# Performance work log

Measured on AMD Instinct MI355X. Metric: run time of the kernel, lower is better.

## Reference

```python
import jax, jax.numpy as jnp
import numpy as np

IN_DIM, OUT_DIM, NUM_KNOTS = 256, 256, 20
X_MIN, X_MAX = -5.0, 5.0
H = (X_MAX - X_MIN) / (NUM_KNOTS - 1)  # uniform knot spacing


def setup_inputs() -> dict:
    key = jax.random.key(0)
    k1, k2 = jax.random.split(key, 2)
    x = jax.random.normal(k1, (1024, IN_DIM), dtype=jnp.float32) * 2.0
    # per-(out,in)-pair cubic coefficients for each of the NUM_KNOTS-1 intervals: [a,b,c,d]
    coeffs = jax.random.normal(k2, (OUT_DIM, IN_DIM, NUM_KNOTS - 1, 4), dtype=jnp.float32) * 0.1
    bias = jnp.zeros((OUT_DIM,), dtype=jnp.float32)
    return {"x": x, "coeffs": coeffs, "bias": bias}


def reference(x, coeffs, bias):
    # x: [B, I]; coeffs: [J, I, K, 4]; bias: [J]
    B, I = x.shape
    K = coeffs.shape[2]
    # locate knot interval (clamped -> linear-cubic extrapolation at edges)
    idx = jnp.clip(jnp.floor((x - X_MIN) / H).astype(jnp.int32), 0, K - 1)  # [B, I]
    t = x - (X_MIN + idx.astype(x.dtype) * H)                               # [B, I]
    # gather per-pair interval coefficients: [J, B, I, 4]
    i_arr = jnp.broadcast_to(jnp.arange(I)[None, :], idx.shape)
    c = coeffs[:, i_arr, idx]
    a, b, c2, d = c[..., 0], c[..., 1], c[..., 2], c[..., 3]
    # Horner evaluation; t broadcasts [B,I] -> [J,B,I]
    y = ((d * t + c2) * t + b) * t + a
    # sum over input dims, add bias: [B, J]
    return y.sum(axis=-1).T + bias[None, :]
```

## Files before the change

### kernel.cpp

```cpp
#include <hip/hip_runtime.h>

#define IN_DIM   256
#define OUT_DIM  256
#define NKNOT    19
#define NCOL     (IN_DIM * NKNOT)
#define CPQ      1216
#define SLICE_U4 (CPQ * 64)
#define X_MIN_C  (-5.0f)
#define H_C      (10.0f / 19.0f)
#define INV_H_C  (19.0f / 10.0f)

typedef __fp16 half2_t __attribute__((ext_vector_type(2)));

__device__ __forceinline__ unsigned int pk_f16(float x, float y) {
    return __builtin_bit_cast(unsigned int, __builtin_amdgcn_cvt_pkrtz(x, y));
}

__device__ __forceinline__ float fdot2(unsigned int w, unsigned int c, float acc) {
#if __has_builtin(__builtin_amdgcn_fdot2)
    return __builtin_amdgcn_fdot2(__builtin_bit_cast(half2_t, w),
                                  __builtin_bit_cast(half2_t, c), acc, false);
#else
    half2_t a = __builtin_bit_cast(half2_t, w);
    half2_t b = __builtin_bit_cast(half2_t, c);
    return acc + (float)a.x * (float)b.x + (float)a.y * (float)b.y;
#endif
}

__global__ __launch_bounds__(256) void transpose_pack(
        const float4* __restrict__ src, uint4* __restrict__ dst) {
    __shared__ uint2 tile[64][65];
    const int c0 = (blockIdx.x % 76) * 64;
    const int r0 = (blockIdx.x / 76) * 64;
    const int tx = threadIdx.x & 63;
    const int ty = threadIdx.x >> 6;

    #pragma unroll
    for (int jj = 0; jj < 16; ++jj) {
        const int r = ty * 16 + jj;
        const float4 v = src[(size_t)(r0 + r) * NCOL + (size_t)(c0 + tx)];
        uint2 p;
        p.x = pk_f16(v.x, v.y);
        p.y = pk_f16(v.z, v.w);
        tile[tx][r] = p;
    }
    __syncthreads();

    const int quarter  = c0 / CPQ;
    const int clbase   = c0 - quarter * CPQ;
    const int o_half   = r0 >> 7;
    const int og2_base = (r0 & 127) >> 1;
    uint4* base = dst + (size_t)(quarter * 2 + o_half) * SLICE_U4;

    #pragma unroll
    for (int jj = 0; jj < 8; ++jj) {
        const int p     = jj * 256 + threadIdx.x;
        const int cl    = p >> 5;
        const int og2l  = p & 31;
        const uint2 t0  = tile[cl][og2l * 2];
        const uint2 t1  = tile[cl][og2l * 2 + 1];
        base[(size_t)(clbase + cl) * 64 + og2_base + og2l] =
            make_uint4(t0.x, t0.y, t1.x, t1.y);
    }
}

__global__ __launch_bounds__(256, 4) void kan_partial(
        const float* __restrict__ x,
        const uint4* __restrict__ Ct,
        float2*      __restrict__ part,
        int B) {
    __shared__ int4 s_tk[4 * 64];

    const int s       = blockIdx.x & 7;
    const int o_half  = s & 1;
    const int quarter = s >> 1;
    const int bgrp    = blockIdx.x >> 3;
    const int tid     = threadIdx.x;

    {
        const int col = tid & 63;
        const int bs  = tid >> 6;
        const float xv = x[(bgrp * 4 + bs) * IN_DIM + quarter * 64 + col];
        const float f  = (xv - X_MIN_C) * INV_H_C;
        int idx = (int)floorf(f);
        idx = idx < 0 ? 0 : (idx > NKNOT - 1 ? NKNOT - 1 : idx);
        const float t  = xv - (X_MIN_C + (float)idx * H_C);
        const float t2 = t * t;
        const float t3 = t2 * t;
        s_tk[bs * 64 + col] = make_int4(idx * 64,
                                        (int)pk_f16(1.0f, t),
                                        (int)pk_f16(t2, t3), 0);
    }
    __syncthreads();

    const int og2 = tid & 63;
    const int bs  = tid >> 6;
    const uint4* base = Ct + (size_t)s * SLICE_U4;
    const int4* tkp = s_tk + bs * 64;

    float y0 = 0.f, y1 = 0.f;

    #pragma unroll 8
    for (int ii = 0; ii < 64; ++ii) {
        const int4 tk = tkp[ii];
        const uint4 Q = base[og2 + ii * 1216 + tk.x];
        const unsigned int w01 = (unsigned int)tk.y;
        const unsigned int w23 = (unsigned int)tk.z;
        y0 = fdot2(w01, Q.x, y0);
        y0 = fdot2(w23, Q.y, y0);
        y1 = fdot2(w01, Q.z, y1);
        y1 = fdot2(w23, Q.w, y1);
    }

    const int b = bgrp * 4 + bs;
    part[(size_t)quarter * (B * 128) + (size_t)b * 128 + o_half * 64 + og2] =
        make_float2(y0, y1);
}

__global__ __launch_bounds__(256) void kan_reduce(
        const float4* __restrict__ part,
        const float4* __restrict__ bias4,
        float4*       __restrict__ out,
        int n4) {
    const int n = blockIdx.x * 256 + threadIdx.x;
    if (n < n4) {
        const float4 p0 = part[n];
        const float4 p1 = part[n4 + n];
        const float4 p2 = part[2 * n4 + n];
        const float4 p3 = part[3 * n4 + n];
        const float4 bv = bias4[n & 63];
        float4 r;
        r.x = (p0.x + p1.x) + (p2.x + p3.x) + bv.x;
        r.y = (p0.y + p1.y) + (p2.y + p3.y) + bv.y;
        r.z = (p0.z + p1.z) + (p2.z + p3.z) + bv.z;
        r.w = (p0.w + p1.w) + (p2.w + p3.w) + bv.w;
        out[n] = r;
    }
}

extern "C" void kernel_launch(void* const* d_in, const int* in_sizes, int n_in,
                              void* d_out, int out_size, void* d_ws, size_t ws_size,
                              hipStream_t stream) {
    const float* x      = (const float*)d_in[0];
    const float* coeffs = (const float*)d_in[1];
    const float* bias   = (const float*)d_in[2];
    float*       out    = (float*)d_out;

    const int B = in_sizes[0] / IN_DIM;
    uint4* Ct   = (uint4*)d_ws;
    float* part = (float*)((char*)d_ws + (16u << 20));

    transpose_pack<<<304, 256, 0, stream>>>((const float4*)coeffs, Ct);

    kan_partial<<<(B / 4) * 8, 256, 0, stream>>>(x, Ct, (float2*)part, B);

    const int n4 = B * OUT_DIM / 4;
    kan_reduce<<<(n4 + 255) / 256, 256, 0, stream>>>(
        (const float4*)part, (const float4*)bias, (float4*)out, n4);
}
```

Baseline: 93.76 us.

## Stage coefficient rows in LDS with double buffering and batch-tile reuse

```diff
diff --git a/kernel.cpp b/kernel.cpp
--- a/kernel.cpp
+++ b/kernel.cpp
@@ -6,6 +6,9 @@
 #define NCOL     (IN_DIM * NKNOT)
 #define CPQ      1216
 #define SLICE_U4 (CPQ * 64)
+#define ROW_U4   1216
+#define NB       128
+#define ISUB     8
 #define X_MIN_C  (-5.0f)
 #define H_C      (10.0f / 19.0f)
 #define INV_H_C  (19.0f / 10.0f)
@@ -64,57 +67,96 @@
     }
 }
 
-__global__ __launch_bounds__(256, 4) void kan_partial(
+__global__ __launch_bounds__(256, 2) void kan_partial(
         const float* __restrict__ x,
         const uint4* __restrict__ Ct,
         float2*      __restrict__ part,
         int B) {
-    __shared__ int4 s_tk[4 * 64];
+    __shared__ int4  s_tk[NB * ISUB];
+    __shared__ uint4 s_cf[2][ROW_U4];
 
     const int s       = blockIdx.x & 7;
+    const int ig      = (blockIdx.x >> 3) & 7;
+    const int bc      = blockIdx.x >> 6;
     const int o_half  = s & 1;
     const int quarter = s >> 1;
-    const int bgrp    = blockIdx.x >> 3;
     const int tid     = threadIdx.x;
+    const int og2     = tid & 63;
+    const int bs      = tid >> 6;
 
-    {
-        const int col = tid & 63;
-        const int bs  = tid >> 6;
-        const float xv = x[(bgrp * 4 + bs) * IN_DIM + quarter * 64 + col];
+    #pragma unroll
+    for (int j = 0; j < (NB * ISUB) / 256; ++j) {
+        const int e  = j * 256 + tid;
+        const int bl = e >> 3;
+        const int il = e & 7;
+        const float xv = x[(size_t)(bc * NB + bl) * IN_DIM + quarter * 64 + ig * ISUB + il];
         const float f  = (xv - X_MIN_C) * INV_H_C;
         int idx = (int)floorf(f);
         idx = idx < 0 ? 0 : (idx > NKNOT - 1 ? NKNOT - 1 : idx);
         const float t  = xv - (X_MIN_C + (float)idx * H_C);
         const float t2 = t * t;
-        const float t3 = t2 * t;
-        s_tk[bs * 64 + col] = make_int4(idx * 64,
-                                        (int)pk_f16(1.0f, t),
-                                        (int)pk_f16(t2, t3), 0);
+        s_tk[e] = make_int4(idx * 64,
+                            (int)pk_f16(1.0f, t),
+                            (int)pk_f16(t2, t2 * t), 0);
+    }
+
+    const uint4* gsrc = Ct + (size_t)s * SLICE_U4 + (size_t)(ig * ISUB) * ROW_U4;
+
+    uint4 ld[5];
+    {
+        const uint4* p = gsrc;
+        #pragma unroll
+        for (int j = 0; j < 4; ++j) ld[j] = p[j * 256 + tid];
+        if (tid < 192) ld[4] = p[1024 + tid];
+        #pragma unroll
+        for (int j = 0; j < 4; ++j) s_cf[0][j * 256 + tid] = ld[j];
+        if (tid < 192) s_cf[0][1024 + tid] = ld[4];
     }
     __syncthreads();
 
-    const int og2 = tid & 63;
-    const int bs  = tid >> 6;
-    const uint4* base = Ct + (size_t)s * SLICE_U4;
-    const int4* tkp = s_tk + bs * 64;
+    float acc0[32], acc1[32];
+    #pragma unroll
+    for (int g = 0; g < 32; ++g) { acc0[g] = 0.f; acc1[g] = 0.f; }
 
-    float y0 = 0.f, y1 = 0.f;
+    for (int il = 0; il < ISUB; ++il) {
+        const int cur = il & 1;
 
-    #pragma unroll 8
-    for (int ii = 0; ii < 64; ++ii) {
-        const int4 tk = tkp[ii];
-        const uint4 Q = base[og2 + ii * 1216 + tk.x];
-        const unsigned int w01 = (unsigned int)tk.y;
-        const unsigned int w23 = (unsigned int)tk.z;
-        y0 = fdot2(w01, Q.x, y0);
-        y0 = fdot2(w23, Q.y, y0);
-        y1 = fdot2(w01, Q.z, y1);
-        y1 = fdot2(w23, Q.w, y1);
+        if (il + 1 < ISUB) {
+            const uint4* p = gsrc + (size_t)(il + 1) * ROW_U4;
+            #pragma unroll
+            for (int j = 0; j < 4; ++j) ld[j] = p[j * 256 + tid];
+            if (tid < 192) ld[4] = p[1024 + tid];
+        }
+
+        #pragma unroll
+        for (int g = 0; g < 32; ++g) {
+            const int  bl = g * 4 + bs;
+            const int4 tk = s_tk[bl * ISUB + il];
+            const uint4 Q = s_cf[cur][tk.x + og2];
+            const unsigned int w01 = (unsigned int)tk.y;
+            const unsigned int w23 = (unsigned int)tk.z;
+            acc0[g] = fdot2(w01, Q.x, acc0[g]);
+            acc0[g] = fdot2(w23, Q.y, acc0[g]);
+            acc1[g] = fdot2(w01, Q.z, acc1[g]);
+            acc1[g] = fdot2(w23, Q.w, acc1[g]);
+        }
+
+        if (il + 1 < ISUB) {
+            const int nxt = cur ^ 1;
+            #pragma unroll
+            for (int j = 0; j < 4; ++j) s_cf[nxt][j * 256 + tid] = ld[j];
+            if (tid < 192) s_cf[nxt][1024 + tid] = ld[4];
+        }
+        __syncthreads();
     }
 
-    const int b = bgrp * 4 + bs;
-    part[(size_t)quarter * (B * 128) + (size_t)b * 128 + o_half * 64 + og2] =
-        make_float2(y0, y1);
+    const int ps = quarter * 8 + ig;
+    #pragma unroll
+    for (int g = 0; g < 32; ++g) {
+        const int b = bc * NB + g * 4 + bs;
+        part[((size_t)ps * B + b) * 128 + o_half * 64 + og2] =
+            make_float2(acc0[g], acc1[g]);
+    }
 }
 
 __global__ __launch_bounds__(256) void kan_reduce(
@@ -123,19 +165,14 @@
         float4*       __restrict__ out,
         int n4) {
     const int n = blockIdx.x * 256 + threadIdx.x;
-    if (n < n4) {
-        const float4 p0 = part[n];
-        const float4 p1 = part[n4 + n];
-        const float4 p2 = part[2 * n4 + n];
-        const float4 p3 = part[3 * n4 + n];
-        const float4 bv = bias4[n & 63];
-        float4 r;
-        r.x = (p0.x + p1.x) + (p2.x + p3.x) + bv.x;
-        r.y = (p0.y + p1.y) + (p2.y + p3.y) + bv.y;
-        r.z = (p0.z + p1.z) + (p2.z + p3.z) + bv.z;
-        r.w = (p0.w + p1.w) + (p2.w + p3.w) + bv.w;
-        out[n] = r;
+    if (n >= n4) return;
+    float4 r = bias4[n & 63];
+    #pragma unroll
+    for (int p = 0; p < 32; ++p) {
+        const float4 v = part[(size_t)p * n4 + n];
+        r.x += v.x; r.y += v.y; r.z += v.z; r.w += v.w;
     }
+    out[n] = r;
 }
 
 extern "C" void kernel_launch(void* const* d_in, const int* in_sizes, int n_in,
@@ -148,11 +185,11 @@
 
     const int B = in_sizes[0] / IN_DIM;
     uint4* Ct   = (uint4*)d_ws;
-    float* part = (float*)((char*)d_ws + (16u << 20));
+    float* part = (float*)((char*)d_ws + (12u << 20));
 
     transpose_pack<<<304, 256, 0, stream>>>((const float4*)coeffs, Ct);
 
-    kan_partial<<<(B / 4) * 8, 256, 0, stream>>>(x, Ct, (float2*)part, B);
+    kan_partial<<<8 * 8 * (B / NB), 256, 0, stream>>>(x, Ct, (float2*)part, B);
 
     const int n4 = B * OUT_DIM / 4;
     kan_reduce<<<(n4 + 255) / 256, 256, 0, stream>>>(
```

After: 134.6 us. +43.6%, slower.

## Store cubic/quadratic coefficients in FP8 with FP16 edge-interval correction pass

Applied to the files above, without the earlier changes.

```diff
diff --git a/kernel.cpp b/kernel.cpp
--- a/kernel.cpp
+++ b/kernel.cpp
@@ -5,15 +5,25 @@
 #define NKNOT    19
 #define NCOL     (IN_DIM * NKNOT)
 #define CPQ      1216
-#define SLICE_U4 (CPQ * 64)
+#define SLICE_E  (CPQ * 64)
+#define EG_SLICE (64 * 2 * 64)
+#define OCAP     32768
 #define X_MIN_C  (-5.0f)
+#define X_MAX_C  (5.0f)
 #define H_C      (10.0f / 19.0f)
 #define INV_H_C  (19.0f / 10.0f)
 
 typedef __fp16 half2_t __attribute__((ext_vector_type(2)));
+typedef float  f32x2  __attribute__((ext_vector_type(2)));
 
 __device__ __forceinline__ unsigned int pk_f16(float x, float y) {
     return __builtin_bit_cast(unsigned int, __builtin_amdgcn_cvt_pkrtz(x, y));
+}
+__device__ __forceinline__ float lo_f16(unsigned int u) {
+    return (float)__builtin_bit_cast(half2_t, u).x;
+}
+__device__ __forceinline__ float hi_f16(unsigned int u) {
+    return (float)__builtin_bit_cast(half2_t, u).y;
 }
 
 __device__ __forceinline__ float fdot2(unsigned int w, unsigned int c, float acc) {
@@ -27,9 +37,64 @@
 #endif
 }
 
+#if __has_builtin(__builtin_amdgcn_cvt_pk_fp8_f32)
+template <bool HI>
+__device__ __forceinline__ unsigned int pk2_fp8(float x, float y, unsigned int old) {
+    return (unsigned int)__builtin_amdgcn_cvt_pk_fp8_f32(x, y, (int)old, HI);
+}
+#else
+__device__ __forceinline__ unsigned int enc1_fp8(float v) {
+    v = fminf(fmaxf(v, -448.f), 448.f);
+    unsigned u = __float_as_uint(v);
+    unsigned s = u >> 31;
+    int e = (int)((u >> 23) & 255) - 127;
+    unsigned m = u & 0x7fffff;
+    if (e < -9) return s << 7;
+    if (e < -6) {
+        unsigned full = m | 0x800000;
+        int sh = 23 - (e + 9);
+        unsigned q = full >> sh, rem = full & ((1u << sh) - 1);
+        q += (rem > (1u << (sh - 1))) || (rem == (1u << (sh - 1)) && (q & 1));
+        return (s << 7) | q;
+    }
+    unsigned q = m >> 20, rem = m & 0xFFFFF;
+    q += (rem > 0x80000) || (rem == 0x80000 && (q & 1));
+    return (s << 7) | ((((unsigned)(e + 7)) << 3) + q);
+}
+template <bool HI>
+__device__ __forceinline__ unsigned int pk2_fp8(float x, float y, unsigned int old) {
+    unsigned p = enc1_fp8(x) | (enc1_fp8(y) << 8);
+    return HI ? ((old & 0xFFFFu) | (p << 16)) : ((old & 0xFFFF0000u) | p);
+}
+#endif
+
+#if __has_builtin(__builtin_amdgcn_cvt_pk_f32_fp8)
+template <bool HI>
+__device__ __forceinline__ f32x2 up2_fp8(unsigned int w) {
+    return __builtin_amdgcn_cvt_pk_f32_fp8((int)w, HI);
+}
+#else
+__device__ __forceinline__ float dec1_fp8(unsigned b) {
+    unsigned s = (b >> 7) & 1, e = (b >> 3) & 15, m = b & 7;
+    float mag = e ? __uint_as_float(((e + 120) << 23) | (m << 20))
+                  : (float)m * 0.001953125f;
+    return s ? -mag : mag;
+}
+template <bool HI>
+__device__ __forceinline__ f32x2 up2_fp8(unsigned int w) {
+    unsigned h = HI ? (w >> 16) : (w & 0xFFFFu);
+    f32x2 r; r.x = dec1_fp8(h & 0xFF); r.y = dec1_fp8(h >> 8);
+    return r;
+}
+#endif
+
 __global__ __launch_bounds__(256) void transpose_pack(
-        const float4* __restrict__ src, uint4* __restrict__ dst) {
-    __shared__ uint2 tile[64][65];
+        const float4* __restrict__ src,
+        uint2* __restrict__ AB, unsigned int* __restrict__ CD,
+        uint2* __restrict__ Eg, int* __restrict__ ocount) {
+    if (blockIdx.x == 0 && threadIdx.x == 0) ocount[0] = 0;
+
+    __shared__ float4 tile[64][65];
     const int c0 = (blockIdx.x % 76) * 64;
     const int r0 = (blockIdx.x / 76) * 64;
     const int tx = threadIdx.x & 63;
@@ -38,11 +103,7 @@
     #pragma unroll
     for (int jj = 0; jj < 16; ++jj) {
         const int r = ty * 16 + jj;
-        const float4 v = src[(size_t)(r0 + r) * NCOL + (size_t)(c0 + tx)];
-        uint2 p;
-        p.x = pk_f16(v.x, v.y);
-        p.y = pk_f16(v.z, v.w);
-        tile[tx][r] = p;
+        tile[tx][r] = src[(size_t)(r0 + r) * NCOL + (size_t)(c0 + tx)];
     }
     __syncthreads();
 
@@ -50,24 +111,44 @@
     const int clbase   = c0 - quarter * CPQ;
     const int o_half   = r0 >> 7;
     const int og2_base = (r0 & 127) >> 1;
-    uint4* base = dst + (size_t)(quarter * 2 + o_half) * SLICE_U4;
+    const int slice    = quarter * 2 + o_half;
+    uint2*        bAB = AB + (size_t)slice * SLICE_E;
+    unsigned int* bCD = CD + (size_t)slice * SLICE_E;
+    uint2*        bEg = Eg + (size_t)slice * EG_SLICE;
 
     #pragma unroll
     for (int jj = 0; jj < 8; ++jj) {
-        const int p     = jj * 256 + threadIdx.x;
-        const int cl    = p >> 5;
-        const int og2l  = p & 31;
-        const uint2 t0  = tile[cl][og2l * 2];
-        const uint2 t1  = tile[cl][og2l * 2 + 1];
-        base[(size_t)(clbase + cl) * 64 + og2_base + og2l] =
-            make_uint4(t0.x, t0.y, t1.x, t1.y);
+        const int p    = jj * 256 + threadIdx.x;
+        const int cl   = p >> 5;
+        const int og2l = p & 31;
+        const float4 v0 = tile[cl][og2l * 2];
+        const float4 v1 = tile[cl][og2l * 2 + 1];
+        uint2 ab;
+        ab.x = pk_f16(v0.x, v0.y);
+        ab.y = pk_f16(v1.x, v1.y);
+        unsigned int cd = pk2_fp8<false>(v0.z, v0.w, 0u);
+        cd = pk2_fp8<true>(v1.z, v1.w, cd);
+        const int colq = clbase + cl;
+        const size_t e = (size_t)colq * 64 + og2_base + og2l;
+        bAB[e] = ab;
+        bCD[e] = cd;
+        const int kk = colq % 19;
+        if (kk == 0 || kk == 18) {
+            const int i_loc = colq / 19;
+            const int ke = kk ? 1 : 0;
+            bEg[(i_loc * 2 + ke) * 64 + og2_base + og2l] =
+                make_uint2(pk_f16(v0.z, v0.w), pk_f16(v1.z, v1.w));
+        }
     }
 }
 
 __global__ __launch_bounds__(256, 4) void kan_partial(
         const float* __restrict__ x,
-        const uint4* __restrict__ Ct,
+        const uint2* __restrict__ AB,
+        const unsigned int* __restrict__ CD,
         float2*      __restrict__ part,
+        int*         __restrict__ ocount,
+        int*         __restrict__ olist,
         int B) {
     __shared__ int4 s_tk[4 * 64];
 
@@ -79,42 +160,95 @@
 
     {
         const int col = tid & 63;
-        const int bs  = tid >> 6;
-        const float xv = x[(bgrp * 4 + bs) * IN_DIM + quarter * 64 + col];
+        const int row = tid >> 6;
+        const int b   = bgrp * 4 + row;
+        const int i   = quarter * 64 + col;
+        const float xv = x[b * IN_DIM + i];
+        const float f  = (xv - X_MIN_C) * INV_H_C;
+        int idx = (int)floorf(f);
+        idx = idx < 0 ? 0 : (idx > NKNOT - 1 ? NKNOT - 1 : idx);
+        const float t  = xv - (X_MIN_C + (float)idx * H_C);
+        const float t2 = t * t;
+        s_tk[row * 64 + col] = make_int4(idx * 64,
+                                        (int)pk_f16(1.0f, t),
+                                        __float_as_int(t2),
+                                        __float_as_int(t2 * t));
+        if (o_half == 0 && (xv < X_MIN_C || xv > X_MAX_C)) {
+            const int slot = atomicAdd(ocount, 1);
+            if (slot < OCAP) olist[slot] = (b << 8) | i;
+        }
+    }
+    __syncthreads();
+
+    const int og2 = tid & 63;
+    const int bs  = tid >> 6;
+    const uint2*        baseAB = AB + (size_t)s * SLICE_E + og2;
+    const unsigned int* baseCD = CD + (size_t)s * SLICE_E + og2;
+    const int4* tkp = s_tk + bs * 64;
+
+    float y0 = 0.f, y1 = 0.f;
+
+    #pragma unroll 8
+    for (int ii = 0; ii < 64; ++ii) {
+        const int4 tk = tkp[ii];
+        const int  e  = ii * 1216 + tk.x;
+        const uint2        ab  = baseAB[e];
+        const unsigned int cdw = baseCD[e];
+        const unsigned int w01 = (unsigned int)tk.y;
+        const float t2 = __int_as_float(tk.z);
+        const float t3 = __int_as_float(tk.w);
+        const f32x2 cd0 = up2_fp8<false>(cdw);
+        const f32x2 cd1 = up2_fp8<true>(cdw);
+        y0 = fdot2(w01, ab.x, y0);
+        y1 = fdot2(w01, ab.y, y1);
+        y0 += cd0.x * t2 + cd0.y * t3;
+        y1 += cd1.x * t2 + cd1.y * t3;
+    }
+
+    const int b = bgrp * 4 + bs;
+    part[(size_t)quarter * (B * 128) + (size_t)b * 128 + o_half * 64 + og2] =
+        make_float2(y0, y1);
+}
+
+__global__ __launch_bounds__(256) void kan_correct(
+        const float* __restrict__ x,
+        const unsigned int* __restrict__ CD,
+        const uint2* __restrict__ Eg,
+        float* __restrict__ part,
+        const int* __restrict__ ocount,
+        const int* __restrict__ olist,
+        int B) {
+    const int half   = threadIdx.x >> 7;
+    const int lt     = threadIdx.x & 127;
+    const int o_half = lt >> 6;
+    const int og2    = lt & 63;
+    const int count  = min(ocount[0], OCAP);
+
+    for (int e = blockIdx.x * 2 + half; e < count; e += gridDim.x * 2) {
+        const int be = olist[e];
+        const int b = be >> 8, i = be & 255;
+        const float xv = x[b * IN_DIM + i];
         const float f  = (xv - X_MIN_C) * INV_H_C;
         int idx = (int)floorf(f);
         idx = idx < 0 ? 0 : (idx > NKNOT - 1 ? NKNOT - 1 : idx);
         const float t  = xv - (X_MIN_C + (float)idx * H_C);
         const float t2 = t * t;
         const float t3 = t2 * t;
-        s_tk[bs * 64 + col] = make_int4(idx * 64,
-                                        (int)pk_f16(1.0f, t),
-                                        (int)pk_f16(t2, t3), 0);
-    }
-    __syncthreads();
-
-    const int og2 = tid & 63;
-    const int bs  = tid >> 6;
-    const uint4* base = Ct + (size_t)s * SLICE_U4;
-    const int4* tkp = s_tk + bs * 64;
-
-    float y0 = 0.f, y1 = 0.f;
-
-    #pragma unroll 8
-    for (int ii = 0; ii < 64; ++ii) {
-        const int4 tk = tkp[ii];
-        const uint4 Q = base[og2 + ii * 1216 + tk.x];
-        const unsigned int w01 = (unsigned int)tk.y;
-        const unsigned int w23 = (unsigned int)tk.z;
-        y0 = fdot2(w01, Q.x, y0);
-        y0 = fdot2(w23, Q.y, y0);
-        y1 = fdot2(w01, Q.z, y1);
-        y1 = fdot2(w23, Q.w, y1);
-    }
-
-    const int b = bgrp * 4 + bs;
-    part[(size_t)quarter * (B * 128) + (size_t)b * 128 + o_half * 64 + og2] =
-        make_float2(y0, y1);
+        const int quarter = i >> 6, i_loc = i & 63;
+        const int ke = idx ? 1 : 0;
+        const int s  = quarter * 2 + o_half;
+        const uint2 cdh = Eg[(size_t)s * EG_SLICE + (i_loc * 2 + ke) * 64 + og2];
+        const unsigned int cdw = CD[(size_t)s * SLICE_E +
+                                    (size_t)(i_loc * 19 + idx) * 64 + og2];
+        const f32x2 q0 = up2_fp8<false>(cdw);
+        const f32x2 q1 = up2_fp8<true>(cdw);
+        const float D0 = (lo_f16(cdh.x) - q0.x) * t2 + (hi_f16(cdh.x) - q0.y) * t3;
+        const float D1 = (lo_f16(cdh.y) - q1.x) * t2 + (hi_f16(cdh.y) - q1.y) * t3;
+        float* pp = part + ((size_t)quarter * (B * 128) +
+                            (size_t)b * 128 + o_half * 64 + og2) * 2;
+        atomicAdd(pp,     D0);
+        atomicAdd(pp + 1, D1);
+    }
 }
 
 __global__ __launch_bounds__(256) void kan_reduce(
@@ -147,12 +281,19 @@
     float*       out    = (float*)d_out;
 
     const int B = in_sizes[0] / IN_DIM;
-    uint4* Ct   = (uint4*)d_ws;
-    float* part = (float*)((char*)d_ws + (16u << 20));
-
-    transpose_pack<<<304, 256, 0, stream>>>((const float4*)coeffs, Ct);
-
-    kan_partial<<<(B / 4) * 8, 256, 0, stream>>>(x, Ct, (float2*)part, B);
+    uint2*        AB   = (uint2*)d_ws;
+    unsigned int* CD   = (unsigned int*)((char*)d_ws + (6u << 20));
+    uint2*        Eg   = (uint2*)((char*)d_ws + (9u << 20));
+    float*        part = (float*)((char*)d_ws + (10u << 20));
+    int*          ocnt = (int*)((char*)d_ws + (14u << 20));
+    int*          olst = ocnt + 16;
+
+    transpose_pack<<<304, 256, 0, stream>>>((const float4*)coeffs, AB, CD, Eg, ocnt);
+
+    kan_partial<<<(B / 4) * 8, 256, 0, stream>>>(x, AB, CD, (float2*)part,
+                                                 ocnt, olst, B);
+
+    kan_correct<<<128, 256, 0, stream>>>(x, CD, Eg, part, ocnt, olst, B);
 
     const int n4 = B * OUT_DIM / 4;
     kan_reduce<<<(n4 + 255) / 256, 256, 0, stream>>>(
```

Result: slower. 137.9 us (+47.1%).
